# Optimization experiments

Measured on AMD Instinct MI355X. Metric: run time of the kernel, lower is better.

## Reference

```python
import jax, jax.numpy as jnp
import numpy as np
import math

NUM_HEADS = 16
HIDDEN = 1024
HEAD_DIM = HIDDEN // NUM_HEADS
MAX_POS = 512
BUCKET = 256
SCALE = 1.0 / math.sqrt(3.0 * HEAD_DIM)


def _make_log_bucket_position(rel_pos):
    # rel_pos: int32 [S, S]
    mid = BUCKET // 2
    rp = rel_pos.astype(jnp.float32)
    sign = jnp.sign(rp)
    abs_pos = jnp.where((rel_pos < mid) & (rel_pos > -mid), float(mid - 1), jnp.abs(rp))
    log_pos = jnp.ceil(jnp.log(abs_pos / mid) * (mid - 1) / math.log((MAX_POS - 1) / mid)) + mid
    bucket_pos = jnp.where(abs_pos <= mid, rp, log_pos * sign)
    return bucket_pos.astype(jnp.int32)


def _get_rel_pos(num_positions):
    ids = jnp.arange(num_positions, dtype=jnp.int32)
    rel_pos = ids[:, None] - ids[None, :]  # [S, S]
    return _make_log_bucket_position(rel_pos)


def setup_inputs() -> dict:
    key = jax.random.key(0)
    ks = jax.random.split(key, 10)
    B, S = 8, 512
    s_in = 1.0 / math.sqrt(HIDDEN)
    inputs = jax.random.normal(ks[0], (B, S, HIDDEN), dtype=jnp.float32)
    rel_embeddings = jax.random.normal(ks[1], (B, 2 * BUCKET, HIDDEN), dtype=jnp.float32)
    Wq = jax.random.normal(ks[2], (HIDDEN, NUM_HEADS, HEAD_DIM), dtype=jnp.float32) * s_in
    Wk = jax.random.normal(ks[3], (HIDDEN, NUM_HEADS, HEAD_DIM), dtype=jnp.float32) * s_in
    Wv = jax.random.normal(ks[4], (HIDDEN, NUM_HEADS, HEAD_DIM), dtype=jnp.float32) * s_in
    bq = jnp.zeros((NUM_HEADS, HEAD_DIM), dtype=jnp.float32)
    bk = jnp.zeros((NUM_HEADS, HEAD_DIM), dtype=jnp.float32)
    bv = jnp.zeros((NUM_HEADS, HEAD_DIM), dtype=jnp.float32)
    Wo = jax.random.normal(ks[5], (HIDDEN, HIDDEN), dtype=jnp.float32) * s_in
    bo = jnp.zeros((HIDDEN,), dtype=jnp.float32)
    return {"inputs": inputs, "rel_embeddings": rel_embeddings,
            "Wq": Wq, "bq": bq, "Wk": Wk, "bk": bk, "Wv": Wv, "bv": bv,
            "Wo": Wo, "bo": bo}


def reference(inputs, rel_embeddings, Wq, bq, Wk, bk, Wv, bv, Wo, bo):
    B, S, _ = inputs.shape
    # projections: [B,S,H,D]
    query = jnp.einsum('bsc,chd->bshd', inputs, Wq) + bq
    key = jnp.einsum('bsc,chd->bshd', inputs, Wk) + bk
    value = jnp.einsum('bsc,chd->bshd', inputs, Wv) + bv

    # content-content scores: [B,H,S_q,S_k]
    scores = jnp.einsum('bkhd,bqhd->bhqk', key, query) * SCALE

    # relative position projections on rel_embeddings [B,P,hidden], P=2*BUCKET
    pos_query = jnp.einsum('bpc,chd->bphd', rel_embeddings, Wq) + bq
    pos_key = jnp.einsum('bpc,chd->bphd', rel_embeddings, Wk) + bk

    rel_pos = _get_rel_pos(S)  # [S,S] int32
    span = BUCKET

    # c2p: query vs pos_key -> [B,H,S,P], gather along last axis
    c2p = jnp.einsum('bphd,bqhd->bhqp', pos_key, query)
    c2p_pos = jnp.clip(rel_pos + span, 0, 2 * span - 1)  # [S,S]
    c2p_idx = jnp.broadcast_to(c2p_pos[None, None], (B, NUM_HEADS, S, S))
    c2p = jnp.take_along_axis(c2p, c2p_idx, axis=3) * SCALE

    # p2c: key vs pos_query -> [B,H,S,P], gather then transpose
    p2c = jnp.einsum('bphd,bkhd->bhkp', pos_query, key)
    p2c_pos = jnp.clip(-rel_pos + span, 0, 2 * span - 1)
    p2c_idx = jnp.broadcast_to(p2c_pos[None, None], (B, NUM_HEADS, S, S))
    p2c = jnp.take_along_axis(p2c, p2c_idx, axis=3)
    p2c = jnp.swapaxes(p2c, 2, 3) * SCALE

    scores = scores + c2p + p2c
    probs = jax.nn.softmax(scores.astype(jnp.float32), axis=-1).astype(inputs.dtype)

    # attend: [B,S,H,D] -> [B,S,hidden]
    attn_out = jnp.einsum('bhqk,bkhd->bqhd', probs, value)
    attn_out = attn_out.reshape(B, S, HIDDEN)
    return jnp.einsum('bsc,cd->bsd', attn_out, Wo) + bo
```

## Files before the change

### kernel.cpp

```cpp
#include <hip/hip_runtime.h>

#define NUM_HEADS 16
#define HEAD_DIM  64
#define HIDDEN    1024
#define SEQ       512
#define BATCH     8
#define NBH       128
#define POSN      512
#define SCALE_F   0.07216878364870323f

typedef __attribute__((ext_vector_type(8))) short  short8;
typedef __attribute__((ext_vector_type(4))) short  short4_t;
typedef __attribute__((ext_vector_type(4))) float  floatx4;

#define GLDS16(gsrc, ldst) \
    __builtin_amdgcn_global_load_lds((const __attribute__((address_space(1))) void*)(gsrc), \
                                     (__attribute__((address_space(3))) void*)(ldst), 16, 0, 0)

__device__ __forceinline__ float bits2f(short s) {
    union { unsigned u; float f; } x;
    x.u = ((unsigned)(unsigned short)s) << 16;
    return x.f;
}
__device__ __forceinline__ short f2bits(float f) {
    union { float f; unsigned u; } x;
    x.f = f;
    unsigned r = x.u + 0x7fffu + ((x.u >> 16) & 1u);
    return (short)(r >> 16);
}

__global__ void conv_pair(const float* __restrict__ a, const float* __restrict__ b,
                          short* __restrict__ oa, short* __restrict__ ob)
{
    const int idx = blockIdx.x * 256 + threadIdx.x;
    floatx4 va = ((const floatx4*)a)[idx];
    floatx4 vb = ((const floatx4*)b)[idx];
    short4_t ra, rb;
#pragma unroll
    for (int i = 0; i < 4; i++) { ra[i] = f2bits(va[i]); rb[i] = f2bits(vb[i]); }
    ((short4_t*)oa)[idx] = ra;
    ((short4_t*)ob)[idx] = rb;
}

__global__ void wtrans(const float* __restrict__ w0, const float* __restrict__ w1,
                       const float* __restrict__ w2, const float* __restrict__ w3,
                       short* __restrict__ o0, short* __restrict__ o1,
                       short* __restrict__ o2, short* __restrict__ o3)
{
    __shared__ float tile[64][65];
    const int z = blockIdx.z;
    const float* src = (z == 0) ? w0 : (z == 1) ? w1 : (z == 2) ? w2 : w3;
    short*       dst = (z == 0) ? o0 : (z == 1) ? o1 : (z == 2) ? o2 : o3;
    const int c0 = blockIdx.x * 64, n0 = blockIdx.y * 64;
    const int t = threadIdx.x;
#pragma unroll
    for (int j = 0; j < 16; j++) {
        const int e = t + j * 256;
        tile[e >> 6][e & 63] = src[(long)(c0 + (e >> 6)) * 1024 + n0 + (e & 63)];
    }
    __syncthreads();
#pragma unroll
    for (int j = 0; j < 16; j++) {
        const int e = t + j * 256;
        dst[(long)(n0 + (e >> 6)) * 1024 + c0 + (e & 63)] = f2bits(tile[e & 63][e >> 6]);
    }
}

__global__ void ftab_build(int* __restrict__ ftab)
{
    const int i = blockIdx.x * 256 + threadIdx.x;
    if (i >= 1023) return;
    const int delta = i - 511;
    const float Cf = (float)log(511.0 / 128.0);
    float absp = (delta < 128 && delta > -128) ? 127.0f : fabsf((float)delta);
    float bucket;
    if (absp <= 128.0f) {
        bucket = (float)delta;
    } else {
        float lp = ceilf((logf(absp * (1.0f / 128.0f)) * 127.0f) / Cf) + 128.0f;
        bucket = (delta > 0) ? lp : -lp;
    }
    int bi = (int)bucket + 256;
    bi = min(max(bi, 0), 511);
    ftab[i] = bi;
}

template<int MODE>
__global__ __launch_bounds__(256)
void gemm_nt(const short* __restrict__ A, long aBatch, int lda,
             const short* __restrict__ BT, long bBatch, int ldb,
             void* __restrict__ O0, void* __restrict__ O1, void* __restrict__ O2,
             long oBatch, int ldo,
             const float* __restrict__ b0, const float* __restrict__ b1,
             const float* __restrict__ b2, int Kd,
             const short* __restrict__ A2,
             void* __restrict__ O3, void* __restrict__ O4)
{
    if (MODE == 6 && blockIdx.z == 1 && blockIdx.y >= 16) return;
    __shared__ __align__(16) short As[128 * 64];
    __shared__ __align__(16) short Bs[128 * 64];
    const int z = blockIdx.z;
    const short* Ab;
    if (MODE == 6 && z == 1) Ab = A2;
    else                     Ab = A + (long)z * aBatch;
    const short* Bb = BT + (long)z * bBatch;
    if (MODE == 6) Bb = BT;
    const int m0 = blockIdx.x * 128, n0 = blockIdx.y * 128;
    const int t = threadIdx.x;
    const int l = t & 63, w = t >> 6;
    const int wm = w >> 1, wn = w & 1;
    const int lr = l & 15, lg = l >> 4;

    floatx4 acc[4][4];
#pragma unroll
    for (int i = 0; i < 4; i++)
#pragma unroll
        for (int j = 0; j < 4; j++) acc[i][j] = (floatx4){0.f, 0.f, 0.f, 0.f};

    for (int k0 = 0; k0 < Kd; k0 += 64) {
        __syncthreads();
#pragma unroll
        for (int j = 0; j < 4; j++) {
            const int c = (w * 4 + j) * 64 + l;
            const int row = c >> 3, pc = c & 7;
            const int cc = pc ^ (row & 7);
            GLDS16(Ab + (long)(m0 + row) * lda + k0 + cc * 8, As + c * 8);
            GLDS16(Bb + (long)(n0 + row) * ldb + k0 + cc * 8, Bs + c * 8);
        }
        __syncthreads();
#pragma unroll
        for (int ks = 0; ks < 2; ks++) {
            short8 af[4], bfr[4];
#pragma unroll
            for (int i = 0; i < 4; i++) {
                const int mr = wm * 64 + i * 16 + lr;
                af[i] = *(const short8*)((char*)As + mr * 128 + (((ks * 4 + lg) ^ (mr & 7)) * 16));
                const int nr = wn * 64 + i * 16 + lr;
                bfr[i] = *(const short8*)((char*)Bs + nr * 128 + (((ks * 4 + lg) ^ (nr & 7)) * 16));
            }
#pragma unroll
            for (int i = 0; i < 4; i++)
#pragma unroll
                for (int j = 0; j < 4; j++)
                    acc[i][j] = __builtin_amdgcn_mfma_f32_16x16x32_bf16(af[i], bfr[j], acc[i][j], 0, 0, 0);
        }
    }

#pragma unroll
    for (int i = 0; i < 4; i++) {
#pragma unroll
        for (int j = 0; j < 4; j++) {
#pragma unroll
            for (int e = 0; e < 4; e++) {
                const int mg = m0 + wm * 64 + i * 16 + lg * 4 + e;
                const int ng = n0 + wn * 64 + j * 16 + lr;
                float v = acc[i][j][e];
                if (MODE == 1) {
                    ((short*)O0)[(long)z * oBatch + (long)mg * ldo + ng] = f2bits(v);
                } else if (MODE == 2) {
                    ((float*)O0)[(long)mg * ldo + ng] = v + b0[ng];
                } else if (MODE == 6) {
                    const int mat = ng >> 10, hh = ng & 1023, h = hh >> 6, d = hh & 63;
                    const int b = mg >> 9, s = mg & 511;
                    v += (mat == 0 ? b0 : mat == 1 ? b1 : b2)[hh];
                    if (z == 0) {
                        short* dst = (short*)(mat == 0 ? O0 : mat == 1 ? O1 : O2);
                        if (mat == 2)
                            dst[((long)(b * NUM_HEADS + h) * HEAD_DIM + d) * SEQ + s] = f2bits(v);
                        else
                            dst[((long)(b * NUM_HEADS + h) * SEQ + s) * HEAD_DIM + d] = f2bits(v);
                    } else {
                        short* dst = (short*)(mat == 0 ? O3 : O4);
                        dst[((long)(b * NUM_HEADS + h) * SEQ + s) * HEAD_DIM + d] = f2bits(v);
                    }
                }
            }
        }
    }
}

__global__ __launch_bounds__(512, 2)
void p2c_fused(const short* __restrict__ posQ, const short* __restrict__ K,
               const int* __restrict__ ftab, short* __restrict__ G)
{
    __shared__ __align__(16) short As[512 * 64];
    __shared__ __align__(16) short Bs[64 * 64];
    __shared__ short ft[1024];
    const int ko = blockIdx.x, bh = blockIdx.y;
    const int k0 = ko * 64;
    const int t = threadIdx.x, l = t & 63, w = t >> 6;
    const int lr = l & 15, lg = l >> 4;
    const short* Ab = posQ + (long)bh * SEQ * HEAD_DIM;
    const short* Kb = K + (long)bh * SEQ * HEAD_DIM;

    for (int i = t; i < 1024; i += 512) ft[i] = (short)((i < 1023) ? ftab[i] : 0);

#pragma unroll
    for (int j = 0; j < 8; j++) {
        const int c = j * 512 + t;
        const int row = c >> 3, pc = c & 7;
        const int cc = pc ^ (row & 7);
        GLDS16(Ab + (long)row * HEAD_DIM + cc * 8, As + c * 8);
    }
    {
        const int c = t;
        const int row = c >> 3, pc = c & 7;
        const int cc = pc ^ (row & 7);
        GLDS16(Kb + (long)(k0 + row) * HEAD_DIM + cc * 8, Bs + c * 8);
    }
    __syncthreads();

    floatx4 acc[4][4];
#pragma unroll
    for (int i = 0; i < 4; i++)
#pragma unroll
        for (int j = 0; j < 4; j++) acc[i][j] = (floatx4){0.f, 0.f, 0.f, 0.f};
#pragma unroll
    for (int ks = 0; ks < 2; ks++) {
        short8 af[4], bfr[4];
#pragma unroll
        for (int i = 0; i < 4; i++) {
            const int mr = w * 64 + i * 16 + lr;
            af[i] = *(const short8*)((char*)As + mr * 128 + (((ks * 4 + lg) ^ (mr & 7)) * 16));
            const int nr = i * 16 + lr;
            bfr[i] = *(const short8*)((char*)Bs + nr * 128 + (((ks * 4 + lg) ^ (nr & 7)) * 16));
        }
#pragma unroll
        for (int i = 0; i < 4; i++)
#pragma unroll
            for (int j = 0; j < 4; j++)
                acc[i][j] = __builtin_amdgcn_mfma_f32_16x16x32_bf16(af[i], bfr[j], acc[i][j], 0, 0, 0);
    }
    __syncthreads();

#pragma unroll
    for (int i = 0; i < 4; i++)
#pragma unroll
        for (int j = 0; j < 4; j++)
#pragma unroll
            for (int e = 0; e < 4; e++) {
                const int p = w * 64 + i * 16 + lg * 4 + e;
                const int kk = j * 16 + lr;
                As[p * 64 + (kk ^ (lg << 4))] = f2bits(acc[i][j][e]);
            }
    __syncthreads();

    short* Gb = G + (long)bh * SEQ * SEQ;
#pragma unroll
    for (int j = 0; j < 8; j++) {
        const int task = j * 512 + t;
        const int q = task >> 3, kc = task & 7;
        short8 v;
#pragma unroll
        for (int i = 0; i < 8; i++) {
            const int kl = kc * 8 + i;
            const int fk = (int)ft[q - (k0 + kl) + 511];
            v[i] = As[fk * 64 + (kl ^ (((fk >> 2) & 3) << 4))];
        }
        *(short8*)(Gb + (long)q * SEQ + k0 + kc * 8) = v;
    }
}

__global__ __launch_bounds__(256, 4)
void attn_fused(const short* __restrict__ Q, const short* __restrict__ K,
                const short* __restrict__ Vt,
                const short* __restrict__ c2pf, const short* __restrict__ Gp2c,
                const int* __restrict__ ftab,
                short* __restrict__ attnO)
{
    __shared__ __align__(16) short c2pS[32 * 512];
    __shared__ float red[2][4][32];
    __shared__ short ft[1024];

    const int lin  = blockIdx.x;
    const int lin2 = (lin & 7) * 256 + (lin >> 3);
    const int bh = lin2 >> 4, qt = lin2 & 15;
    const int q0 = qt * 32;
    const int t = threadIdx.x, l = t & 63, w = t >> 6;
    const int lr = l & 15, lg = l >> 4;
    const long pbase = (long)bh * SEQ * HEAD_DIM;
    const short* Qb  = Q  + pbase;
    const short* Kb  = K  + pbase;
    const short* Vtb = Vt + pbase;
    const short* c2pb = c2pf + (long)bh * SEQ * POSN;
    const short* Gb   = Gp2c + (long)bh * SEQ * SEQ;

    for (int i = t; i < 1024; i += 256) ft[i] = (short)((i < 1023) ? ftab[i] : 0);

#pragma unroll
    for (int j = 0; j < 8; j++) {
        const int c = w * 512 + j * 64 + l;
        const int row = c >> 6, cc = c & 63;
        GLDS16(c2pb + (long)(q0 + row) * POSN + (cc ^ (row & 7)) * 8, c2pS + c * 8);
    }

    short8 aq[2][2];
#pragma unroll
    for (int mt = 0; mt < 2; mt++)
#pragma unroll
        for (int ks = 0; ks < 2; ks++)
            aq[mt][ks] = *(const short8*)(Qb + (q0 + mt * 16 + lr) * 64 + ks * 32 + lg * 8);

    floatx4 acc[2][8];
#pragma unroll
    for (int mt = 0; mt < 2; mt++)
#pragma unroll
        for (int nt = 0; nt < 8; nt++) acc[mt][nt] = (floatx4){0.f, 0.f, 0.f, 0.f};

#pragma unroll
    for (int nt = 0; nt < 8; nt++) {
        const int kr = w * 128 + nt * 16 + lr;
        short8 kb0 = *(const short8*)(Kb + kr * 64 + lg * 8);
        short8 kb1 = *(const short8*)(Kb + kr * 64 + 32 + lg * 8);
#pragma unroll
        for (int mt = 0; mt < 2; mt++) {
            acc[mt][nt] = __builtin_amdgcn_mfma_f32_16x16x32_bf16(aq[mt][0], kb0, acc[mt][nt], 0, 0, 0);
            acc[mt][nt] = __builtin_amdgcn_mfma_f32_16x16x32_bf16(aq[mt][1], kb1, acc[mt][nt], 0, 0, 0);
        }
    }

    __syncthreads();

#pragma unroll
    for (int mt = 0; mt < 2; mt++)
#pragma unroll
        for (int nt = 0; nt < 8; nt++) {
            const int k = w * 128 + nt * 16 + lr;
#pragma unroll
            for (int e = 0; e < 4; e++) {
                const int r = mt * 16 + lg * 4 + e;
                const int fk = (int)ft[q0 + r - k + 511];
                acc[mt][nt][e] = (acc[mt][nt][e]
                                  + bits2f(c2pS[r * 512 + (fk ^ ((r & 7) << 3))])
                                  + bits2f(Gb[(long)(q0 + r) * SEQ + k])) * SCALE_F;
            }
        }

#pragma unroll
    for (int mt = 0; mt < 2; mt++)
#pragma unroll
        for (int e = 0; e < 4; e++) {
            float m = acc[mt][0][e];
#pragma unroll
            for (int nt = 1; nt < 8; nt++) m = fmaxf(m, acc[mt][nt][e]);
            m = fmaxf(m, __shfl_xor(m, 1));
            m = fmaxf(m, __shfl_xor(m, 2));
            m = fmaxf(m, __shfl_xor(m, 4));
            m = fmaxf(m, __shfl_xor(m, 8));
            red[0][w][mt * 16 + lg * 4 + e] = m;
        }
    __syncthreads();

#pragma unroll
    for (int mt = 0; mt < 2; mt++)
#pragma unroll
        for (int e = 0; e < 4; e++) {
            const int r = mt * 16 + lg * 4 + e;
            const float m = fmaxf(fmaxf(red[0][0][r], red[0][1][r]),
                                  fmaxf(red[0][2][r], red[0][3][r]));
            float s = 0.f;
#pragma unroll
            for (int nt = 0; nt < 8; nt++) {
                float p = __expf(acc[mt][nt][e] - m);
                acc[mt][nt][e] = p;
                s += p;
            }
            s += __shfl_xor(s, 1); s += __shfl_xor(s, 2);
            s += __shfl_xor(s, 4); s += __shfl_xor(s, 8);
            red[1][w][r] = s;
#pragma unroll
            for (int nt = 0; nt < 8; nt++) {
                const int kcol = w * 128 + nt * 16 + lr;
                int byte = r * 1024 + kcol * 2;
                byte ^= (r & 7) << 4;
                *(short*)((char*)c2pS + byte) = f2bits(acc[mt][nt][e]);
            }
        }
    __syncthreads();

    floatx4 accO[2];
    accO[0] = (floatx4){0.f, 0.f, 0.f, 0.f};
    accO[1] = (floatx4){0.f, 0.f, 0.f, 0.f};
#pragma unroll
    for (int ks = 0; ks < 16; ks++) {
        short8 vb = *(const short8*)(Vtb + (long)(w * 16 + lr) * SEQ + ks * 32 + lg * 8);
#pragma unroll
        for (int mt = 0; mt < 2; mt++) {
            const int qr = mt * 16 + lr;
            int byte = qr * 1024 + (ks * 32 + lg * 8) * 2;
            byte ^= (qr & 7) << 4;
            short8 pa = *(const short8*)((char*)c2pS + byte);
            accO[mt] = __builtin_amdgcn_mfma_f32_16x16x32_bf16(pa, vb, accO[mt], 0, 0, 0);
        }
    }

    const int b = bh >> 4, h = bh & 15;
#pragma unroll
    for (int mt = 0; mt < 2; mt++)
#pragma unroll
        for (int e = 0; e < 4; e++) {
            const int r = mt * 16 + lg * 4 + e;
            const float rs = red[1][0][r] + red[1][1][r] + red[1][2][r] + red[1][3][r];
            const float v = accO[mt][e] / rs;
            attnO[((long)(b * SEQ + q0 + r)) * HIDDEN + h * HEAD_DIM + w * 16 + lr] = f2bits(v);
        }
}

extern "C" void kernel_launch(void* const* d_in, const int* in_sizes, int n_in,
                              void* d_out, int out_size, void* d_ws, size_t ws_size,
                              hipStream_t stream)
{
    const float* inputs = (const float*)d_in[0];
    const float* rel    = (const float*)d_in[1];
    const float* Wq     = (const float*)d_in[2];
    const float* bq     = (const float*)d_in[3];
    const float* Wk     = (const float*)d_in[4];
    const float* bk     = (const float*)d_in[5];
    const float* Wv     = (const float*)d_in[6];
    const float* bv     = (const float*)d_in[7];
    const float* Wo     = (const float*)d_in[8];
    const float* bo     = (const float*)d_in[9];
    float* out = (float*)d_out;

    char* ws = (char*)d_ws;
    size_t off = 0;
    auto alloc = [&](size_t bytes) -> char* {
        char* p = ws + off;
        off += (bytes + 255) & ~(size_t)255;
        return p;
    };
    short* inA   = (short*)alloc(4194304ull * 2);
    short* inRel = (short*)alloc(4194304ull * 2);
    short* WqT   = (short*)alloc(1048576ull * 2);
    short* WkT   = (short*)alloc(1048576ull * 2);
    short* WvT   = (short*)alloc(1048576ull * 2);
    short* WoT   = (short*)alloc(1048576ull * 2);
    short* Qw    = (short*)alloc(4194304ull * 2);
    short* Kw    = (short*)alloc(4194304ull * 2);
    short* Vtw   = (short*)alloc(4194304ull * 2);
    short* posQw = (short*)alloc(4194304ull * 2);
    short* posKw = (short*)alloc(4194304ull * 2);
    short* c2pW  = (short*)alloc(33554432ull * 2);
    short* GW    = (short*)alloc(33554432ull * 2);
    short* attnW = (short*)alloc(4194304ull * 2);
    int*   ftabW = (int*)alloc(4096);

    conv_pair<<<4096, 256, 0, stream>>>(inputs, rel, inA, inRel);
    wtrans<<<dim3(16, 16, 4), 256, 0, stream>>>(Wq, Wk, Wv, Wo, WqT, WkT, WvT, WoT);
    ftab_build<<<4, 256, 0, stream>>>(ftabW);

    gemm_nt<6><<<dim3(32, 24, 2), 256, 0, stream>>>(inA, 0, 1024, WqT, 0, 1024,
                                                    Qw, Kw, Vtw, 0, 0, bq, bk, bv, 1024,
                                                    inRel, posQw, posKw);

    gemm_nt<1><<<dim3(4, 4, 128), 256, 0, stream>>>(Qw, 32768, 64, posKw, 32768, 64,
                                                    c2pW, nullptr, nullptr, 262144, 512,
                                                    nullptr, nullptr, nullptr, 64,
                                                    nullptr, nullptr, nullptr);

    p2c_fused<<<dim3(8, 128), 512, 0, stream>>>(posQw, Kw, ftabW, GW);

    attn_fused<<<2048, 256, 0, stream>>>(Qw, Kw, Vtw, c2pW, GW, ftabW, attnW);

    gemm_nt<2><<<dim3(32, 8), 256, 0, stream>>>(attnW, 0, 1024, WoT, 0, 1024,
                                                out, nullptr, nullptr, 0, 1024, bo, nullptr, nullptr, 1024,
                                                nullptr, nullptr, nullptr);
}
```

Before: 218.3 us.

## Double-buffer GEMM LDS tiles, remap projection grid, and stage transposed V stores

The generic NT GEMM now double-buffers its A/B LDS tiles so global-to-LDS loads of the next K slice overlap the MFMA work on the current one. The fused projection launch replaces the 3D grid, which contained idle blocks, with a compact 32x40 linear grid plus a swizzled tile mapping. The transposed V output is now staged through LDS so it can be written with coalesced 16-byte stores instead of scattered 2-byte ones. The cost is doubled shared memory (64KB per block), which may lower occupancy for every GEMM mode.

```diff
diff --git a/kernel.cpp b/kernel.cpp
--- a/kernel.cpp
+++ b/kernel.cpp
@@ -96,16 +96,34 @@
              const short* __restrict__ A2,
              void* __restrict__ O3, void* __restrict__ O4)
 {
-    if (MODE == 6 && blockIdx.z == 1 && blockIdx.y >= 16) return;
-    __shared__ __align__(16) short As[128 * 64];
-    __shared__ __align__(16) short Bs[128 * 64];
+    __shared__ __align__(16) short As[2][128 * 64];
+    __shared__ __align__(16) short Bs[2][128 * 64];
+
+    int m0, n0, yy = 0;
+    bool z1 = false;
     const int z = blockIdx.z;
+    if (MODE == 6) {
+        const int lin = blockIdx.x + (blockIdx.y << 5);
+        const int swz = (lin & 7) * 160 + (lin >> 3);
+        m0 = (swz & 31) * 128;
+        yy = swz >> 5;
+        z1 = (yy >= 24);
+        n0 = (z1 ? (yy - 24) : yy) * 128;
+    } else {
+        m0 = blockIdx.x * 128;
+        n0 = blockIdx.y * 128;
+    }
+
     const short* Ab;
-    if (MODE == 6 && z == 1) Ab = A2;
-    else                     Ab = A + (long)z * aBatch;
-    const short* Bb = BT + (long)z * bBatch;
-    if (MODE == 6) Bb = BT;
-    const int m0 = blockIdx.x * 128, n0 = blockIdx.y * 128;
+    const short* Bb;
+    if (MODE == 6) {
+        Ab = z1 ? A2 : A;
+        Bb = BT;
+    } else {
+        Ab = A + (long)z * aBatch;
+        Bb = BT + (long)z * bBatch;
+    }
+
     const int t = threadIdx.x;
     const int l = t & 63, w = t >> 6;
     const int wm = w >> 1, wn = w & 1;
@@ -117,26 +135,38 @@
 #pragma unroll
         for (int j = 0; j < 4; j++) acc[i][j] = (floatx4){0.f, 0.f, 0.f, 0.f};
 
-    for (int k0 = 0; k0 < Kd; k0 += 64) {
-        __syncthreads();
-#pragma unroll
-        for (int j = 0; j < 4; j++) {
-            const int c = (w * 4 + j) * 64 + l;
-            const int row = c >> 3, pc = c & 7;
-            const int cc = pc ^ (row & 7);
-            GLDS16(Ab + (long)(m0 + row) * lda + k0 + cc * 8, As + c * 8);
-            GLDS16(Bb + (long)(n0 + row) * ldb + k0 + cc * 8, Bs + c * 8);
-        }
-        __syncthreads();
+#pragma unroll
+    for (int j = 0; j < 4; j++) {
+        const int c = (w * 4 + j) * 64 + l;
+        const int row = c >> 3, pc = c & 7;
+        const int cc = pc ^ (row & 7);
+        GLDS16(Ab + (long)(m0 + row) * lda + cc * 8, As[0] + c * 8);
+        GLDS16(Bb + (long)(n0 + row) * ldb + cc * 8, Bs[0] + c * 8);
+    }
+    __syncthreads();
+
+    int cur = 0;
+    for (int k0 = 0; k0 < Kd; k0 += 64, cur ^= 1) {
+        if (k0 + 64 < Kd) {
+            const int kn = k0 + 64;
+#pragma unroll
+            for (int j = 0; j < 4; j++) {
+                const int c = (w * 4 + j) * 64 + l;
+                const int row = c >> 3, pc = c & 7;
+                const int cc = pc ^ (row & 7);
+                GLDS16(Ab + (long)(m0 + row) * lda + kn + cc * 8, As[cur ^ 1] + c * 8);
+                GLDS16(Bb + (long)(n0 + row) * ldb + kn + cc * 8, Bs[cur ^ 1] + c * 8);
+            }
+        }
 #pragma unroll
         for (int ks = 0; ks < 2; ks++) {
             short8 af[4], bfr[4];
 #pragma unroll
             for (int i = 0; i < 4; i++) {
                 const int mr = wm * 64 + i * 16 + lr;
-                af[i] = *(const short8*)((char*)As + mr * 128 + (((ks * 4 + lg) ^ (mr & 7)) * 16));
+                af[i] = *(const short8*)((char*)As[cur] + mr * 128 + (((ks * 4 + lg) ^ (mr & 7)) * 16));
                 const int nr = wn * 64 + i * 16 + lr;
-                bfr[i] = *(const short8*)((char*)Bs + nr * 128 + (((ks * 4 + lg) ^ (nr & 7)) * 16));
+                bfr[i] = *(const short8*)((char*)Bs[cur] + nr * 128 + (((ks * 4 + lg) ^ (nr & 7)) * 16));
             }
 #pragma unroll
             for (int i = 0; i < 4; i++)
@@ -144,6 +174,35 @@
                 for (int j = 0; j < 4; j++)
                     acc[i][j] = __builtin_amdgcn_mfma_f32_16x16x32_bf16(af[i], bfr[j], acc[i][j], 0, 0, 0);
         }
+        __syncthreads();
+    }
+
+    if (MODE == 6 && !z1 && yy >= 16) {
+        short* tp = &As[0][0];
+#pragma unroll
+        for (int i = 0; i < 4; i++)
+#pragma unroll
+            for (int j = 0; j < 4; j++)
+#pragma unroll
+                for (int e = 0; e < 4; e++) {
+                    const int ml  = wm * 64 + i * 16 + lg * 4 + e;
+                    const int ngl = wn * 64 + j * 16 + lr;
+                    const float v = acc[i][j][e] + b2[(n0 & 1023) + ngl];
+                    tp[ngl * 128 + (ml ^ ((ngl & 7) << 4))] = f2bits(v);
+                }
+        __syncthreads();
+        const int b = m0 >> 9, s0 = m0 & 511;
+        const int hb = (n0 & 1023) >> 6;
+        short* dst = (short*)O2;
+#pragma unroll
+        for (int j = 0; j < 8; j++) {
+            const int task = t + j * 256;
+            const int r = task >> 4, c = task & 15;
+            short8 v8 = *(const short8*)(tp + r * 128 + ((c * 8) ^ ((r & 7) << 4)));
+            const int h = hb + (r >> 6), d = r & 63;
+            *(short8*)(dst + ((long)((b * NUM_HEADS + h) * HEAD_DIM + d)) * SEQ + s0 + c * 8) = v8;
+        }
+        return;
     }
 
 #pragma unroll
@@ -160,19 +219,14 @@
                 } else if (MODE == 2) {
                     ((float*)O0)[(long)mg * ldo + ng] = v + b0[ng];
                 } else if (MODE == 6) {
-                    const int mat = ng >> 10, hh = ng & 1023, h = hh >> 6, d = hh & 63;
+                    const int hh = ng & 1023, mat = ng >> 10;
+                    const int h = hh >> 6, d = hh & 63;
                     const int b = mg >> 9, s = mg & 511;
-                    v += (mat == 0 ? b0 : mat == 1 ? b1 : b2)[hh];
-                    if (z == 0) {
-                        short* dst = (short*)(mat == 0 ? O0 : mat == 1 ? O1 : O2);
-                        if (mat == 2)
-                            dst[((long)(b * NUM_HEADS + h) * HEAD_DIM + d) * SEQ + s] = f2bits(v);
-                        else
-                            dst[((long)(b * NUM_HEADS + h) * SEQ + s) * HEAD_DIM + d] = f2bits(v);
-                    } else {
-                        short* dst = (short*)(mat == 0 ? O3 : O4);
-                        dst[((long)(b * NUM_HEADS + h) * SEQ + s) * HEAD_DIM + d] = f2bits(v);
-                    }
+                    v += (mat == 0 ? b0 : b1)[hh];
+                    short* dst;
+                    if (z1) dst = (short*)(mat == 0 ? O3 : O4);
+                    else    dst = (short*)(mat == 0 ? O0 : O1);
+                    dst[((long)(b * NUM_HEADS + h) * SEQ + s) * HEAD_DIM + d] = f2bits(v);
                 }
             }
         }
@@ -449,9 +503,9 @@
     wtrans<<<dim3(16, 16, 4), 256, 0, stream>>>(Wq, Wk, Wv, Wo, WqT, WkT, WvT, WoT);
     ftab_build<<<4, 256, 0, stream>>>(ftabW);
 
-    gemm_nt<6><<<dim3(32, 24, 2), 256, 0, stream>>>(inA, 0, 1024, WqT, 0, 1024,
-                                                    Qw, Kw, Vtw, 0, 0, bq, bk, bv, 1024,
-                                                    inRel, posQw, posKw);
+    gemm_nt<6><<<dim3(32, 40), 256, 0, stream>>>(inA, 0, 1024, WqT, 0, 1024,
+                                                 Qw, Kw, Vtw, 0, 0, bq, bk, bv, 1024,
+                                                 inRel, posQw, posKw);
 
     gemm_nt<1><<<dim3(4, 4, 128), 256, 0, stream>>>(Qw, 32768, 64, posKw, 32768, 64,
                                                     c2pW, nullptr, nullptr, 262144, 512,
```

Measured after the change: 204.6 us. 1.07x faster.
